# Kernel tuning notes

Measured on AMD Instinct MI355X. Metric: run time of the kernel, lower is better.

Reference implementation:

```python
import jax, jax.numpy as jnp
import numpy as np

N_NODES = 20000
N_EDGES = 320000
F_IN = 64      # num_node_features
C = 64         # out_features (per-head channels, concat=False)
H = 4          # n_heads
L = 3          # n_layers (stackable since F_IN == C)
N_RES = 2
N_PAIRS = 8192
EDGE_DIM = 9
HID = 64 * C   # ResNetGated hidden dim = 64 * out_features
N_EXPERTS = 8


def setup_inputs() -> dict:
    key = jax.random.key(0)
    ks = jax.random.split(key, 24)
    s = 0.05
    f32 = jnp.float32
    inp = {}
    inp["x"] = jax.random.normal(ks[0], (N_NODES, F_IN), f32)
    inp["edge_index"] = jax.random.randint(ks[1], (2, N_EDGES), 0, N_NODES)
    inp["edge_attr"] = jax.random.normal(ks[2], (N_EDGES, EDGE_DIM), f32)
    inp["edge_cross"] = jax.random.randint(ks[3], (N_PAIRS, 2), 0, N_NODES)
    inp["types"] = jax.random.randint(ks[4], (N_PAIRS,), 0, N_EXPERTS)
    # GATv2 encoder params, stacked over L layers (layer 0 in-dim == C)
    inp["gat_Wl"] = jax.random.normal(ks[5], (L, F_IN, H * C), f32) * s
    inp["gat_bl"] = jnp.full((L, H * C), 0.01, f32)
    inp["gat_Wr"] = jax.random.normal(ks[6], (L, F_IN, H * C), f32) * s
    inp["gat_br"] = jnp.full((L, H * C), 0.01, f32)
    inp["gat_We"] = jax.random.normal(ks[7], (L, EDGE_DIM, H * C), f32) * s  # lin_edge, no bias
    inp["gat_att"] = jax.random.normal(ks[8], (L, H, C), f32) * s
    inp["gat_bias"] = jnp.zeros((L, C), f32)
    inp["gat_gates"] = jax.random.normal(ks[9], (L,), f32) * 0.5
    # 8 type-routed experts: ResNetGated(2C -> 64C -> 2C) x N_RES, then Linear(2C, 1)
    inp["res_W1"] = jax.random.normal(ks[10], (N_EXPERTS, N_RES, 2 * C, HID), f32) * s
    inp["res_b1"] = jnp.full((N_EXPERTS, N_RES, HID), 0.01, f32)
    inp["res_W2"] = jax.random.normal(ks[11], (N_EXPERTS, N_RES, HID, 2 * C), f32) * s
    inp["res_b2"] = jnp.full((N_EXPERTS, N_RES, 2 * C), 0.01, f32)
    inp["res_gates"] = jax.random.normal(ks[12], (N_EXPERTS, N_RES), f32) * 0.5
    inp["head_W"] = jax.random.normal(ks[13], (N_EXPERTS, 2 * C, 1), f32) * s
    inp["head_b"] = jnp.full((N_EXPERTS, 1), 0.01, f32)
    return inp


def _gat_layer(h, src, tgt, ea, Wl, bl, Wr, br, We, att, bias):
    # GATv2Conv with edge features, concat=False (mean over heads)
    n = h.shape[0]
    nh, c = att.shape
    xl = (h @ Wl + bl).reshape(n, nh, c)   # source transform (x_j)
    xr = (h @ Wr + br).reshape(n, nh, c)   # target transform (x_i)
    e = (ea @ We).reshape(-1, nh, c)
    m = jax.nn.leaky_relu(xl[src] + xr[tgt] + e, 0.2)       # [E,H,C]
    logits = jnp.einsum('ehc,hc->eh', m, att)               # [E,H]
    mx = jax.ops.segment_max(logits, tgt, num_segments=n)
    a = jnp.exp(logits - mx[tgt])
    den = jax.ops.segment_sum(a, tgt, num_segments=n)
    alpha = a / den[tgt]                                     # segment softmax over in-edges
    out = jax.ops.segment_sum(xl[src] * alpha[:, :, None], tgt, num_segments=n)
    return out.mean(axis=1) + bias


def reference(x, edge_index, edge_attr, edge_cross, types,
              gat_Wl, gat_bl, gat_Wr, gat_br, gat_We, gat_att, gat_bias, gat_gates,
              res_W1, res_b1, res_W2, res_b2, res_gates, head_W, head_b):
    src, tgt = edge_index[0], edge_index[1]
    g = jax.nn.sigmoid(gat_gates)
    h = _gat_layer(x, src, tgt, edge_attr, gat_Wl[0], gat_bl[0], gat_Wr[0], gat_br[0],
                   gat_We[0], gat_att[0], gat_bias[0])
    for i in range(1, gat_Wl.shape[0]):
        h = jax.nn.leaky_relu(h, 0.01)
        hi = _gat_layer(h, src, tgt, edge_attr, gat_Wl[i], gat_bl[i], gat_Wr[i], gat_br[i],
                        gat_We[i], gat_att[i], gat_bias[i])
        h = g[i - 1] * hi + (1 - g[i - 1]) * h
    # pair gather + feature interleave: x[edge_cross].transpose(1,2).reshape(P, 2C)
    pair = h[edge_cross]                               # [P,2,C]
    p = pair.shape[0]
    z0 = jnp.swapaxes(pair, 1, 2).reshape(p, -1)        # [P,2C]
    outs = []
    for e in range(res_W1.shape[0]):
        z = z0
        ge = jax.nn.sigmoid(res_gates[e])
        for r in range(res_W1.shape[1]):
            z = jax.nn.relu(z)
            y = jax.nn.relu(z @ res_W1[e, r] + res_b1[e, r]) @ res_W2[e, r] + res_b2[e, r]
            z = ge[r] * y + (1 - ge[r]) * z
        outs.append(z @ head_W[e] + head_b[e])          # [P,1]
    all_out = jnp.stack(outs)                           # [8,P,1]
    per_row = all_out[types, jnp.arange(p)]             # [P,1] per-row expert output
    order = jnp.argsort(types, stable=True)             # concat groups type 0..7, stable in-group
    return per_row[order]
```

## Files before the change

### kernel.cpp

```cpp
#include <hip/hip_runtime.h>

#define NN 20000
#define NE 320000
#define NL 3
#define NP 8192
#define EDIM 9
#define TROWS 32
#define MAXT 272
#define CAPR (MAXT*TROWS)
#define NB ((NN+255)/256)

typedef _Float16 f16x8 __attribute__((ext_vector_type(8)));
typedef float f32x4 __attribute__((ext_vector_type(4)));

#define GLL16(g,l) __builtin_amdgcn_global_load_lds((const __attribute__((address_space(1))) unsigned int*)(g), (__attribute__((address_space(3))) unsigned int*)(l), 16, 0, 0)

__device__ __forceinline__ float sigm(float x){ return 1.f/(1.f+__expf(-x)); }

__device__ __forceinline__ float dpp_sum64(float x){
  x += __int_as_float(__builtin_amdgcn_update_dpp(0, __float_as_int(x), 0x111, 0xf, 0xf, true));
  x += __int_as_float(__builtin_amdgcn_update_dpp(0, __float_as_int(x), 0x112, 0xf, 0xf, true));
  x += __int_as_float(__builtin_amdgcn_update_dpp(0, __float_as_int(x), 0x114, 0xf, 0xf, true));
  x += __int_as_float(__builtin_amdgcn_update_dpp(0, __float_as_int(x), 0x118, 0xf, 0xf, true));
  x += __int_as_float(__builtin_amdgcn_update_dpp(0, __float_as_int(x), 0x142, 0xf, 0xf, true));
  x += __int_as_float(__builtin_amdgcn_update_dpp(0, __float_as_int(x), 0x143, 0xf, 0xf, true));
  return __uint_as_float(__builtin_amdgcn_readlane(__float_as_uint(x), 63));
}

__global__ void k_deg(const int* __restrict__ ei, int* __restrict__ deg){
  int e=blockIdx.x*blockDim.x+threadIdx.x; if(e<NE) atomicAdd(&deg[ei[NE+e]],1);
}

__global__ __launch_bounds__(256) void k_scan1(const int* __restrict__ deg, int* __restrict__ incl, int* __restrict__ bsum){
  __shared__ int sh[256];
  int b=blockIdx.x, tid=threadIdx.x;
  int i=b*256+tid;
  int v=(i<NN)?deg[i]:0;
  sh[tid]=v; __syncthreads();
  for(int o=1;o<256;o<<=1){
    int t=(tid>=o)?sh[tid-o]:0; __syncthreads();
    sh[tid]+=t; __syncthreads();
  }
  if(i<NN) incl[i]=sh[tid];
  if(tid==255) bsum[b]=sh[255];
}
__global__ __launch_bounds__(256) void k_scan3(const int* __restrict__ deg, const int* __restrict__ incl,
                        const int* __restrict__ bsum, int* __restrict__ row_ptr, int* __restrict__ cursor){
  __shared__ int sh[256];
  int b=blockIdx.x, tid=threadIdx.x;
  sh[tid]=(tid<b && tid<NB)?bsum[tid]:0;
  __syncthreads();
  for(int o=128;o>0;o>>=1){ if(tid<o) sh[tid]+=sh[tid+o]; __syncthreads(); }
  int boff=sh[0];
  int i=b*256+tid;
  if(i<NN){
    int r=incl[i]+boff;
    row_ptr[i+1]=r; cursor[i]=r-deg[i];
  }
  if(i==0) row_ptr[0]=0;
}

__global__ void k_fill_csr2(const int* __restrict__ ei, const float* __restrict__ ea,
    int* __restrict__ cursor, int* __restrict__ csr_src, float* __restrict__ eas){
  int e=blockIdx.x*blockDim.x+threadIdx.x;
  if(e<NE){
    int t=ei[NE+e]; int pos=atomicAdd(&cursor[t],1);
    csr_src[pos]=ei[e];
    const float* s=ea+(size_t)e*9;
    float* d=eas+(size_t)pos*12;
    #pragma unroll
    for(int k=0;k<9;++k) d[k]=s[k];
    d[9]=0.f; d[10]=0.f; d[11]=0.f;
  }
}

__global__ __launch_bounds__(256) void k_sort(const int* __restrict__ types, int* __restrict__ meta,
    int* __restrict__ slotp, int* __restrict__ islot){
  __shared__ int cnt[256][8];
  __shared__ int tot[8];
  __shared__ int base_s[8], pad_s[8];
  int tid=threadIdx.x;
  int lc[8]={0,0,0,0,0,0,0,0};
  int tl[32];
  for(int i=0;i<32;++i){ int ty=types[tid*32+i]; tl[i]=ty; lc[ty]++; }
  #pragma unroll
  for(int t=0;t<8;++t) cnt[tid][t]=lc[t];
  __syncthreads();
  if(tid<8){
    int run=0;
    for(int j=0;j<256;++j){ int v=cnt[j][tid]; cnt[j][tid]=run; run+=v; }
    tot[tid]=run;
  }
  __syncthreads();
  if(tid==0){
    int b=0, pb=0, nt=0;
    for(int t=0;t<8;++t){
      base_s[t]=b; pad_s[t]=pb;
      meta[t]=tot[t]; meta[8+t]=b; meta[16+t]=pb;
      int ntt=(tot[t]+31)>>5;
      for(int j=0;j<ntt;++j){ meta[32+nt]=t; meta[32+MAXT+nt]=pb+j*32; nt++; }
      b+=tot[t]; pb+=ntt*32;
    }
    meta[24]=nt; meta[25]=pb;
  }
  __syncthreads();
  if(tid<8){
    int t=tid; int ntt=(tot[t]+31)>>5;
    for(int sr=tot[t]; sr<ntt*32; ++sr) islot[pad_s[t]+sr]=-1;
  }
  int run[8];
  #pragma unroll
  for(int t=0;t<8;++t) run[t]=cnt[tid][t];
  for(int i=0;i<32;++i){
    int p=tid*32+i; int t=tl[i]; int r=run[t]++;
    int pos=base_s[t]+r, slot=pad_s[t]+r;
    slotp[p]=slot; islot[slot]=pos;
  }
}

__global__ __launch_bounds__(256) void k_nodexf(const float* __restrict__ hin,
    const float* __restrict__ Wl, const float* __restrict__ bl,
    const float* __restrict__ Wr, const float* __restrict__ br,
    float* __restrict__ xl, float* __restrict__ xr, int lk){
  __shared__ float hsT[64][68];
  __shared__ float ws[64][68];
  int bid=blockIdx.x;
  int n0=(bid>>3)*64, ch=bid&7;
  const float* W=(ch<4)?Wl:Wr;
  const float* bb=(ch<4)?bl:br;
  float* outp=(ch<4)?xl:xr;
  int c0=(ch&3)*64;
  int tid=threadIdx.x;

  for(int idx=tid; idx<64*16; idx+=256){
    int r=idx&63, kq=idx>>6;
    int n=n0+r;
    float4 v=make_float4(0.f,0.f,0.f,0.f);
    if(n<NN) v=*(const float4*)&hin[(size_t)n*64+kq*4];
    if(lk){
      v.x=v.x>0.f?v.x:0.01f*v.x; v.y=v.y>0.f?v.y:0.01f*v.y;
      v.z=v.z>0.f?v.z:0.01f*v.z; v.w=v.w>0.f?v.w:0.01f*v.w;
    }
    hsT[kq*4+0][r]=v.x; hsT[kq*4+1][r]=v.y; hsT[kq*4+2][r]=v.z; hsT[kq*4+3][r]=v.w;
  }
  for(int idx=tid; idx<64*16; idx+=256){
    int k=idx>>4, j4=idx&15;
    *(float4*)&ws[k][j4*4]=*(const float4*)&W[(size_t)k*256+c0+j4*4];
  }
  __syncthreads();

  int ty=tid>>4, tx=tid&15;
  float acc[4][4]={};
  #pragma unroll 4
  for(int k=0;k<64;++k){
    float4 a=*(const float4*)&hsT[k][4*ty];
    float4 b=*(const float4*)&ws[k][4*tx];
    float aa[4]={a.x,a.y,a.z,a.w}, bbv[4]={b.x,b.y,b.z,b.w};
    #pragma unroll
    for(int i=0;i<4;++i){
      #pragma unroll
      for(int j=0;j<4;++j) acc[i][j]=fmaf(aa[i],bbv[j],acc[i][j]);
    }
  }
  float4 bias4=*(const float4*)&bb[c0+4*tx];
  #pragma unroll
  for(int i=0;i<4;++i){
    int n=n0+4*ty+i;
    if(n<NN){
      float4 o=make_float4(acc[i][0]+bias4.x, acc[i][1]+bias4.y, acc[i][2]+bias4.z, acc[i][3]+bias4.w);
      *(float4*)&outp[(size_t)n*256+c0+4*tx]=o;
    }
  }
}

__global__ __launch_bounds__(256) void k_agg2(const float* __restrict__ xl, const float* __restrict__ xr,
    const float* __restrict__ eas, const int* __restrict__ csr_src, const int* __restrict__ row_ptr,
    const float* __restrict__ WeL, const float* __restrict__ attL,
    const float* __restrict__ biasL, const float* __restrict__ gates, int layer,
    const float* __restrict__ hprev, float* __restrict__ hout){
  __shared__ float red[4][64];
  int n=blockIdx.x, tid=threadIdx.x;
  float w0=WeL[tid],      w1=WeL[256+tid],  w2=WeL[512+tid],  w3=WeL[768+tid],  w4=WeL[1024+tid];
  float w5=WeL[1280+tid], w6=WeL[1536+tid], w7=WeL[1792+tid], w8=WeL[2048+tid];
  float att_t=attL[tid];
  float xr_t=xr[(size_t)n*256+tid];
  int s=row_ptr[n], t=row_ptr[n+1];
  float den=0.f, acc=0.f;

  auto body=[&](float xlv, int j){
    const float4* ep=(const float4*)(eas+(size_t)j*12);
    float4 e0=ep[0], e1=ep[1];
    float e8=eas[(size_t)j*12+8];
    float ev=e0.x*w0+e0.y*w1+e0.z*w2+e0.w*w3+e1.x*w4+e1.y*w5+e1.z*w6+e1.w*w7+e8*w8;
    float m=xlv+xr_t+ev;
    m=m>0.f?m:0.2f*m;
    float pt=dpp_sum64(m*att_t);
    float a=__expf(pt);
    den+=a; acc+=a*xlv;
  };

  float x0=0.f,x1=0.f,x2=0.f,x3=0.f;
  if(s+0<t) x0=xl[(size_t)csr_src[s+0]*256+tid];
  if(s+1<t) x1=xl[(size_t)csr_src[s+1]*256+tid];
  if(s+2<t) x2=xl[(size_t)csr_src[s+2]*256+tid];
  if(s+3<t) x3=xl[(size_t)csr_src[s+3]*256+tid];
  int j=s;
  while(j+7<t){
    float y0=xl[(size_t)csr_src[j+4]*256+tid];
    float y1=xl[(size_t)csr_src[j+5]*256+tid];
    float y2=xl[(size_t)csr_src[j+6]*256+tid];
    float y3=xl[(size_t)csr_src[j+7]*256+tid];
    body(x0,j); body(x1,j+1); body(x2,j+2); body(x3,j+3);
    x0=y0; x1=y1; x2=y2; x3=y3;
    j+=4;
  }
  if(j<t){ body(x0,j); ++j; }
  if(j<t){ body(x1,j); ++j; }
  if(j<t){ body(x2,j); ++j; }
  if(j<t){ body(x3,j); ++j; }
  while(j<t){ body(xl[(size_t)csr_src[j]*256+tid], j); ++j; }

  float rdn=den>0.f?1.f/den:0.f;
  int h=tid>>6, cc=tid&63;
  red[h][cc]=acc*rdn;
  __syncthreads();
  if(tid<64){
    float mean=(red[0][tid]+red[1][tid]+red[2][tid]+red[3][tid])*0.25f + biasL[tid];
    float o;
    if(layer==0) o=mean;
    else{
      float hp=hprev[(size_t)n*64+tid];
      hp=hp>0.f?hp:0.01f*hp;
      float g=sigm(gates[layer-1]);
      o=g*mean+(1.f-g)*hp;
    }
    hout[(size_t)n*64+tid]=o;
  }
}

__global__ void k_buildz(const float* __restrict__ hfin, const int* __restrict__ ecross,
    const int* __restrict__ slotp, float* __restrict__ z){
  int g=blockIdx.x*blockDim.x+threadIdx.x;
  if(g>=NP*64) return;
  int p=g>>6, c=g&63;
  int a=ecross[2*p], b=ecross[2*p+1];
  int slot=slotp[p];
  float2 v; v.x=hfin[(size_t)a*64+c]; v.y=hfin[(size_t)b*64+c];
  ((float2*)(z+(size_t)slot*128))[c]=v;
}

__global__ __launch_bounds__(256) void k_prepw1(const float* __restrict__ src, _Float16* __restrict__ dst){
  __shared__ float lds[128][33];
  int bid=blockIdx.x, er=bid>>7, ch=bid&127;
  const float* s=src+(size_t)er*128*4096 + ch*32;
  int tid=threadIdx.x;
  for(int idx=tid; idx<128*32; idx+=256){ int k=idx>>5, jl=idx&31; lds[k][jl]=s[(size_t)k*4096+jl]; }
  __syncthreads();
  _Float16* d=dst+(size_t)bid*4096;
  for(int g=tid; g<512; g+=256){
    int jl=g>>4, k8=g&15;
    f16x8 v;
    #pragma unroll
    for(int t=0;t<8;++t) v[t]=(_Float16)lds[k8*8+t][jl];
    int elem=(jl*128+k8*8)^((jl&7)<<3);
    *(f16x8*)(&d[elem])=v;
  }
}

__global__ __launch_bounds__(256) void k_prepw2(const float* __restrict__ src, _Float16* __restrict__ dst){
  __shared__ float lds[32][130];
  int bid=blockIdx.x, er=bid>>7, ch=bid&127;
  const float* s=src+(size_t)er*4096*128 + (size_t)ch*32*128;
  int tid=threadIdx.x;
  for(int idx=tid; idx<32*128; idx+=256){ int j=idx>>7, n=idx&127; lds[j][n]=s[(size_t)j*128+n]; }
  __syncthreads();
  _Float16* d=dst+(size_t)bid*4096;
  for(int g=tid; g<512; g+=256){
    int n=g>>2, j8=g&3;
    f16x8 v;
    #pragma unroll
    for(int t=0;t<8;++t) v[t]=(_Float16)lds[j8*8+t][n];
    int elem=(n*32+j8*8)^((n&7)<<3);
    *(f16x8*)(&d[elem])=v;
  }
}

__global__ __launch_bounds__(256) void k_resmfma(const float* __restrict__ zin,
    const _Float16* __restrict__ w1t, const _Float16* __restrict__ w2t,
    const float* __restrict__ b1all, const int* __restrict__ meta,
    float* __restrict__ ypart, int rb)
{
  __shared__ _Float16 zh[32*128];
  __shared__ _Float16 wb[2][8192];
  __shared__ _Float16 ts[2][32*32];
  __shared__ float b1s[1024];
  int bidl=blockIdx.x;
  int bid=(bidl&7)*132+(bidl>>3);
  int v=bid>>2, hq=bid&3;
  int nt=meta[24];
  if(v>=nt) return;
  int e=meta[32+v], row0=meta[32+MAXT+v];
  int er=e*2+rb;
  const _Float16* w1b=w1t+(size_t)er*524288 + (size_t)hq*32*4096;
  const _Float16* w2b=w2t+(size_t)er*524288 + (size_t)hq*32*4096;
  const float* b1g=b1all+(size_t)er*4096 + hq*1024;
  int tid=threadIdx.x, l=tid&63, w=tid>>6;
  int lm=l&15, lq=l>>4;
  int s16=(w&1)*16, jh=w>>1;
  int arow=s16+lm;

  for(int g=tid; g<512; g+=256){
    int row=g>>4, slot=g&15;
    const float* src=zin+(size_t)(row0+row)*128+slot*8;
    float4 v0=*(const float4*)src;
    float4 v1=*(const float4*)(src+4);
    f16x8 hv;
    hv[0]=(_Float16)fmaxf(v0.x,0.f); hv[1]=(_Float16)fmaxf(v0.y,0.f);
    hv[2]=(_Float16)fmaxf(v0.z,0.f); hv[3]=(_Float16)fmaxf(v0.w,0.f);
    hv[4]=(_Float16)fmaxf(v1.x,0.f); hv[5]=(_Float16)fmaxf(v1.y,0.f);
    hv[6]=(_Float16)fmaxf(v1.z,0.f); hv[7]=(_Float16)fmaxf(v1.w,0.f);
    *(f16x8*)(&zh[(row*128+slot*8)^((row&7)<<3)])=hv;
  }
  for(int g=tid; g<1024; g+=256) b1s[g]=b1g[g];

  #pragma unroll
  for(int s=0;s<2;++s){
    int so=(w*2+s)*512;
    GLL16(w1b+so+l*8, &wb[0][so]);
    GLL16(w2b+so+l*8, &wb[0][4096+so]);
  }
  asm volatile("s_waitcnt lgkmcnt(0)" ::: "memory");
  __builtin_amdgcn_sched_barrier(0);
  __builtin_amdgcn_s_barrier();

  f32x4 yacc[4];
  #pragma unroll
  for(int i=0;i<4;++i){ yacc[i][0]=0.f; yacc[i][1]=0.f; yacc[i][2]=0.f; yacc[i][3]=0.f; }

  for(int cc=0; cc<32; ++cc){
    int buf=cc&1;
    asm volatile("s_waitcnt vmcnt(0)" ::: "memory");
    __builtin_amdgcn_sched_barrier(0);
    __builtin_amdgcn_s_barrier();
    if(cc<31){
      const _Float16* g1=w1b+(size_t)(cc+1)*4096;
      const _Float16* g2=w2b+(size_t)(cc+1)*4096;
      int nb=buf^1;
      #pragma unroll
      for(int s=0;s<2;++s){
        int so=(w*2+s)*512;
        GLL16(g1+so+l*8, &wb[nb][so]);
        GLL16(g2+so+l*8, &wb[nb][4096+so]);
      }
    }

    f32x4 tacc={0.f,0.f,0.f,0.f};
    int j=jh*16+lm;
    #pragma unroll
    for(int ks=0;ks<4;++ks){
      f16x8 a=*(const f16x8*)(&zh[(arow*128+ks*32+lq*8)^((arow&7)<<3)]);
      f16x8 b=*(const f16x8*)(&wb[buf][(j*128+ks*32+lq*8)^((j&7)<<3)]);
      tacc=__builtin_amdgcn_mfma_f32_16x16x32_f16(a,b,tacc,0,0,0);
    }
    float b1v=b1s[cc*32+j];
    #pragma unroll
    for(int r=0;r<4;++r){
      int trow=s16+lq*4+r;
      ts[buf][(trow*32+j)^((trow&7)<<3)]=(_Float16)fmaxf(tacc[r]+b1v,0.f);
    }
    asm volatile("s_waitcnt lgkmcnt(0)" ::: "memory");
    __builtin_amdgcn_sched_barrier(0);
    __builtin_amdgcn_s_barrier();

    f16x8 a2=*(const f16x8*)(&ts[buf][(arow*32+lq*8)^((arow&7)<<3)]);
    #pragma unroll
    for(int nf=0;nf<4;++nf){
      int n=jh*64+nf*16+lm;
      f16x8 b=*(const f16x8*)(&wb[buf][4096+((n*32+lq*8)^((n&7)<<3))]);
      yacc[nf]=__builtin_amdgcn_mfma_f32_16x16x32_f16(a2,b,yacc[nf],0,0,0);
    }
  }

  float* yp=ypart+(size_t)hq*CAPR*128;
  #pragma unroll
  for(int nf=0;nf<4;++nf){
    int col=jh*64+nf*16+lm;
    #pragma unroll
    for(int r=0;r<4;++r)
      yp[(size_t)(row0+s16+lq*4+r)*128+col]=yacc[nf][r];
  }
}

__global__ __launch_bounds__(256) void k_comb(const float* __restrict__ zin, const float* __restrict__ ypart,
    const float* __restrict__ b2all, const float* __restrict__ gates, const int* __restrict__ meta,
    int rb, float* __restrict__ zout,
    const float* __restrict__ hWg, const float* __restrict__ hbg, const int* __restrict__ islot,
    float* __restrict__ out)
{
  int v=blockIdx.x;
  if(v>=meta[24]) return;
  int e=meta[32+v], row0=meta[32+MAXT+v];
  int er=e*2+rb;
  float ge=sigm(gates[er]);
  const float* b2=b2all+(size_t)er*128;
  int tid=threadIdx.x;
  const size_t HS=(size_t)CAPR*128;
  if(rb==0){
    for(int idx=tid; idx<32*128; idx+=256){
      int r=idx>>7, c=idx&127;
      size_t o=(size_t)(row0+r)*128+c;
      float y=ypart[o]+ypart[HS+o]+ypart[2*HS+o]+ypart[3*HS+o];
      float zr=fmaxf(zin[o],0.f);
      zout[o]=ge*(y+b2[c])+(1.f-ge)*zr;
    }
  }else{
    int r=tid>>3, cs=tid&7;
    float acc=0.f;
    size_t ro=(size_t)(row0+r)*128;
    #pragma unroll
    for(int q=0;q<16;++q){
      int c=cs*16+q;
      size_t o=ro+c;
      float y=ypart[o]+ypart[HS+o]+ypart[2*HS+o]+ypart[3*HS+o];
      float zr=fmaxf(zin[o],0.f);
      float zf=ge*(y+b2[c])+(1.f-ge)*zr;
      acc+=zf*hWg[e*128+c];
    }
    acc+=__shfl_xor(acc,1); acc+=__shfl_xor(acc,2); acc+=__shfl_xor(acc,4);
    if(cs==0){
      int pos=islot[row0+r];
      if(pos>=0) out[pos]=acc+hbg[e];
    }
  }
}

extern "C" void kernel_launch(void* const* d_in, const int* in_sizes, int n_in,
                              void* d_out, int out_size, void* d_ws, size_t ws_size,
                              hipStream_t stream){
  const float* x     =(const float*)d_in[0];
  const int*   ei    =(const int*)  d_in[1];
  const float* ea    =(const float*)d_in[2];
  const int*   ecross=(const int*)  d_in[3];
  const int*   types =(const int*)  d_in[4];
  const float* gWl   =(const float*)d_in[5];
  const float* gbl   =(const float*)d_in[6];
  const float* gWr   =(const float*)d_in[7];
  const float* gbr   =(const float*)d_in[8];
  const float* gWe   =(const float*)d_in[9];
  const float* gatt  =(const float*)d_in[10];
  const float* gbias =(const float*)d_in[11];
  const float* ggate =(const float*)d_in[12];
  const float* rW1   =(const float*)d_in[13];
  const float* rb1   =(const float*)d_in[14];
  const float* rW2   =(const float*)d_in[15];
  const float* rb2   =(const float*)d_in[16];
  const float* rg    =(const float*)d_in[17];
  const float* hW    =(const float*)d_in[18];
  const float* hb    =(const float*)d_in[19];
  float* out=(float*)d_out;

  char* base=(char*)d_ws;
  size_t off=0;
  auto alloc=[&](size_t bytes)->char*{
    char* p=base+off;
    off=(off+bytes+511)&~((size_t)511);
    return p;
  };
  float* hA     =(float*)alloc((size_t)NN*64*4);
  float* hB     =(float*)alloc((size_t)NN*64*4);
  int*   deg    =(int*)  alloc((size_t)NN*4);
  int*   row_ptr=(int*)  alloc((size_t)(NN+1)*4);
  int*   cursor =(int*)  alloc((size_t)NN*4);
  int*   incl   =(int*)  alloc((size_t)NN*4);
  int*   bsum   =(int*)  alloc(256*4);
  int*   csr_src=(int*)  alloc((size_t)(NE+16)*4);
  int*   meta   =(int*)  alloc(1024*4);
  int*   slotp  =(int*)  alloc((size_t)NP*4);
  int*   islot  =(int*)  alloc((size_t)CAPR*4);
  float* zA     =(float*)alloc((size_t)CAPR*128*4);
  size_t uoff=off;
  float* xl =(float*)(base+uoff);
  float* xr =(float*)(base+uoff+(size_t)NN*256*4);
  float* eas=(float*)(base+uoff+(size_t)NN*256*4*2);
  _Float16* w1t=(_Float16*)(base+uoff);
  _Float16* w2t=(_Float16*)(base+uoff+(size_t)16*524288*2);
  float* ypart =(float*)(base+uoff+(size_t)16*524288*2*2);
  size_t gat_bytes=(size_t)NN*256*4*2 + (size_t)(NE*12+16)*4;
  size_t exp_bytes=(size_t)16*524288*2*2 + (size_t)4*CAPR*128*4;
  size_t need=uoff+(gat_bytes>exp_bytes?gat_bytes:exp_bytes);
  if(ws_size<need) return;
  float* zB=hB;

  hipMemsetAsync(deg,0,(size_t)NN*4,stream);
  k_deg<<<(NE+255)/256,256,0,stream>>>(ei,deg);
  k_scan1<<<NB,256,0,stream>>>(deg,incl,bsum);
  k_scan3<<<NB,256,0,stream>>>(deg,incl,bsum,row_ptr,cursor);
  k_fill_csr2<<<(NE+255)/256,256,0,stream>>>(ei,ea,cursor,csr_src,eas);
  k_sort<<<1,256,0,stream>>>(types,meta,slotp,islot);

  const float* hcur=x;
  float* hnext=hA;
  for(int L=0;L<NL;++L){
    k_nodexf<<<((NN+63)/64)*8,256,0,stream>>>(hcur, gWl+(size_t)L*64*256, gbl+(size_t)L*256,
                                              gWr+(size_t)L*64*256, gbr+(size_t)L*256, xl, xr, L>0?1:0);
    k_agg2<<<NN,256,0,stream>>>(xl,xr,eas,csr_src,row_ptr, gWe+(size_t)L*EDIM*256,
                                gatt+(size_t)L*256, gbias+(size_t)L*64, ggate, L, hcur, hnext);
    hcur=hnext;
    hnext=(hcur==hA)?hB:hA;
  }

  k_buildz<<<NP*64/256,256,0,stream>>>(hcur,ecross,slotp,zA);

  k_prepw1<<<2048,256,0,stream>>>(rW1,w1t);
  k_prepw2<<<2048,256,0,stream>>>(rW2,w2t);

  k_resmfma<<<1056,256,0,stream>>>(zA,w1t,w2t,rb1,meta,ypart,0);
  k_comb<<<MAXT,256,0,stream>>>(zA,ypart,rb2,rg,meta,0,zB,hW,hb,islot,out);
  k_resmfma<<<1056,256,0,stream>>>(zB,w1t,w2t,rb1,meta,ypart,1);
  k_comb<<<MAXT,256,0,stream>>>(zB,ypart,rb2,rg,meta,1,zA,hW,hb,islot,out);

  (void)in_sizes; (void)n_in; (void)out_size;
}
```

Baseline: 550.2 us.

## Triple-buffer expert weight loads and merge prep kernels into one launch

The expert MLP MFMA kernel now keeps three LDS weight buffers and prefetches two chunks ahead, waiting with a partial vmcnt so the previous prefetch stays in flight. This is meant to hide global-to-LDS latency better than strict double buffering. The weight transpose/convert kernels and the pair-gather kernel are fused into a single launch to cut launch overhead. The larger LDS footprint may lower occupancy of the MFMA kernel.

After: 573.9 us. 1.04x slower.

```diff
diff --git a/kernel.cpp b/kernel.cpp
--- a/kernel.cpp
+++ b/kernel.cpp
@@ -238,50 +238,47 @@
   }
 }
 
-__global__ void k_buildz(const float* __restrict__ hfin, const int* __restrict__ ecross,
+__global__ __launch_bounds__(256) void k_prep_all(const float* __restrict__ rW1, _Float16* __restrict__ w1t,
+    const float* __restrict__ rW2, _Float16* __restrict__ w2t,
+    const float* __restrict__ hfin, const int* __restrict__ ecross,
     const int* __restrict__ slotp, float* __restrict__ z){
-  int g=blockIdx.x*blockDim.x+threadIdx.x;
-  if(g>=NP*64) return;
-  int p=g>>6, c=g&63;
-  int a=ecross[2*p], b=ecross[2*p+1];
-  int slot=slotp[p];
-  float2 v; v.x=hfin[(size_t)a*64+c]; v.y=hfin[(size_t)b*64+c];
-  ((float2*)(z+(size_t)slot*128))[c]=v;
-}
-
-__global__ __launch_bounds__(256) void k_prepw1(const float* __restrict__ src, _Float16* __restrict__ dst){
-  __shared__ float lds[128][33];
-  int bid=blockIdx.x, er=bid>>7, ch=bid&127;
-  const float* s=src+(size_t)er*128*4096 + ch*32;
-  int tid=threadIdx.x;
-  for(int idx=tid; idx<128*32; idx+=256){ int k=idx>>5, jl=idx&31; lds[k][jl]=s[(size_t)k*4096+jl]; }
-  __syncthreads();
-  _Float16* d=dst+(size_t)bid*4096;
-  for(int g=tid; g<512; g+=256){
-    int jl=g>>4, k8=g&15;
-    f16x8 v;
-    #pragma unroll
-    for(int t=0;t<8;++t) v[t]=(_Float16)lds[k8*8+t][jl];
-    int elem=(jl*128+k8*8)^((jl&7)<<3);
-    *(f16x8*)(&d[elem])=v;
-  }
-}
-
-__global__ __launch_bounds__(256) void k_prepw2(const float* __restrict__ src, _Float16* __restrict__ dst){
-  __shared__ float lds[32][130];
-  int bid=blockIdx.x, er=bid>>7, ch=bid&127;
-  const float* s=src+(size_t)er*4096*128 + (size_t)ch*32*128;
-  int tid=threadIdx.x;
-  for(int idx=tid; idx<32*128; idx+=256){ int j=idx>>7, n=idx&127; lds[j][n]=s[(size_t)j*128+n]; }
-  __syncthreads();
-  _Float16* d=dst+(size_t)bid*4096;
-  for(int g=tid; g<512; g+=256){
-    int n=g>>2, j8=g&3;
-    f16x8 v;
-    #pragma unroll
-    for(int t=0;t<8;++t) v[t]=(_Float16)lds[j8*8+t][n];
-    int elem=(n*32+j8*8)^((n&7)<<3);
-    *(f16x8*)(&d[elem])=v;
+  __shared__ float lds[128*33];
+  int bigbid=blockIdx.x, tid=threadIdx.x;
+  if(bigbid<2048){
+    int bid=bigbid, er=bid>>7, ch=bid&127;
+    const float* s=rW1+(size_t)er*128*4096 + ch*32;
+    for(int idx=tid; idx<128*32; idx+=256){ int k=idx>>5, jl=idx&31; lds[k*33+jl]=s[(size_t)k*4096+jl]; }
+    __syncthreads();
+    _Float16* d=w1t+(size_t)bid*4096;
+    for(int g=tid; g<512; g+=256){
+      int jl=g>>4, k8=g&15;
+      f16x8 v;
+      #pragma unroll
+      for(int t=0;t<8;++t) v[t]=(_Float16)lds[(k8*8+t)*33+jl];
+      int elem=(jl*128+k8*8)^((jl&7)<<3);
+      *(f16x8*)(&d[elem])=v;
+    }
+  }else if(bigbid<4096){
+    int bid=bigbid-2048, er=bid>>7, ch=bid&127;
+    const float* s=rW2+(size_t)er*4096*128 + (size_t)ch*32*128;
+    for(int idx=tid; idx<32*128; idx+=256){ int j=idx>>7, n=idx&127; lds[j*130+n]=s[(size_t)j*128+n]; }
+    __syncthreads();
+    _Float16* d=w2t+(size_t)bid*4096;
+    for(int g=tid; g<512; g+=256){
+      int n=g>>2, j8=g&3;
+      f16x8 v;
+      #pragma unroll
+      for(int t=0;t<8;++t) v[t]=(_Float16)lds[(j8*8+t)*130+n];
+      int elem=(n*32+j8*8)^((n&7)<<3);
+      *(f16x8*)(&d[elem])=v;
+    }
+  }else{
+    int g=(bigbid-4096)*256+tid;
+    int p=g>>6, c=g&63;
+    int a=ecross[2*p], b=ecross[2*p+1];
+    int slot=slotp[p];
+    float2 v; v.x=hfin[(size_t)a*64+c]; v.y=hfin[(size_t)b*64+c];
+    ((float2*)(z+(size_t)slot*128))[c]=v;
   }
 }
 
@@ -291,7 +288,7 @@
     float* __restrict__ ypart, int rb)
 {
   __shared__ _Float16 zh[32*128];
-  __shared__ _Float16 wb[2][8192];
+  __shared__ _Float16 wb[3][8192];
   __shared__ _Float16 ts[2][32*32];
   __shared__ float b1s[1024];
   int bidl=blockIdx.x;
@@ -329,6 +326,16 @@
     GLL16(w1b+so+l*8, &wb[0][so]);
     GLL16(w2b+so+l*8, &wb[0][4096+so]);
   }
+  {
+    const _Float16* g1=w1b+4096;
+    const _Float16* g2=w2b+4096;
+    #pragma unroll
+    for(int s=0;s<2;++s){
+      int so=(w*2+s)*512;
+      GLL16(g1+so+l*8, &wb[1][so]);
+      GLL16(g2+so+l*8, &wb[1][4096+so]);
+    }
+  }
   asm volatile("s_waitcnt lgkmcnt(0)" ::: "memory");
   __builtin_amdgcn_sched_barrier(0);
   __builtin_amdgcn_s_barrier();
@@ -337,20 +344,20 @@
   #pragma unroll
   for(int i=0;i<4;++i){ yacc[i][0]=0.f; yacc[i][1]=0.f; yacc[i][2]=0.f; yacc[i][3]=0.f; }
 
+  int buf=0, tb=2;
   for(int cc=0; cc<32; ++cc){
-    int buf=cc&1;
-    asm volatile("s_waitcnt vmcnt(0)" ::: "memory");
+    if(cc<31){ asm volatile("s_waitcnt vmcnt(4)" ::: "memory"); }
+    else     { asm volatile("s_waitcnt vmcnt(0)" ::: "memory"); }
     __builtin_amdgcn_sched_barrier(0);
     __builtin_amdgcn_s_barrier();
-    if(cc<31){
-      const _Float16* g1=w1b+(size_t)(cc+1)*4096;
-      const _Float16* g2=w2b+(size_t)(cc+1)*4096;
-      int nb=buf^1;
+    if(cc<30){
+      const _Float16* g1=w1b+(size_t)(cc+2)*4096;
+      const _Float16* g2=w2b+(size_t)(cc+2)*4096;
       #pragma unroll
       for(int s=0;s<2;++s){
         int so=(w*2+s)*512;
-        GLL16(g1+so+l*8, &wb[nb][so]);
-        GLL16(g2+so+l*8, &wb[nb][4096+so]);
+        GLL16(g1+so+l*8, &wb[tb][so]);
+        GLL16(g2+so+l*8, &wb[tb][4096+so]);
       }
     }
 
@@ -363,22 +370,25 @@
       tacc=__builtin_amdgcn_mfma_f32_16x16x32_f16(a,b,tacc,0,0,0);
     }
     float b1v=b1s[cc*32+j];
+    int tbuf=cc&1;
     #pragma unroll
     for(int r=0;r<4;++r){
       int trow=s16+lq*4+r;
-      ts[buf][(trow*32+j)^((trow&7)<<3)]=(_Float16)fmaxf(tacc[r]+b1v,0.f);
+      ts[tbuf][(trow*32+j)^((trow&7)<<3)]=(_Float16)fmaxf(tacc[r]+b1v,0.f);
     }
     asm volatile("s_waitcnt lgkmcnt(0)" ::: "memory");
     __builtin_amdgcn_sched_barrier(0);
     __builtin_amdgcn_s_barrier();
 
-    f16x8 a2=*(const f16x8*)(&ts[buf][(arow*32+lq*8)^((arow&7)<<3)]);
+    f16x8 a2=*(const f16x8*)(&ts[tbuf][(arow*32+lq*8)^((arow&7)<<3)]);
     #pragma unroll
     for(int nf=0;nf<4;++nf){
       int n=jh*64+nf*16+lm;
       f16x8 b=*(const f16x8*)(&wb[buf][4096+((n*32+lq*8)^((n&7)<<3))]);
       yacc[nf]=__builtin_amdgcn_mfma_f32_16x16x32_f16(a2,b,yacc[nf],0,0,0);
     }
+    buf=(buf==2)?0:buf+1;
+    tb =(tb ==2)?0:tb +1;
   }
 
   float* yp=ypart+(size_t)hq*CAPR*128;
@@ -509,10 +519,7 @@
     hnext=(hcur==hA)?hB:hA;
   }
 
-  k_buildz<<<NP*64/256,256,0,stream>>>(hcur,ecross,slotp,zA);
-
-  k_prepw1<<<2048,256,0,stream>>>(rW1,w1t);
-  k_prepw2<<<2048,256,0,stream>>>(rW2,w2t);
+  k_prep_all<<<6144,256,0,stream>>>(rW1,w1t,rW2,w2t,hcur,ecross,slotp,zA);
 
   k_resmfma<<<1056,256,0,stream>>>(zA,w1t,w2t,rb1,meta,ypart,0);
   k_comb<<<MAXT,256,0,stream>>>(zA,ypart,rb2,rg,meta,0,zB,hW,hb,islot,out);
```
